# Kernel optimization log

Measured on AMD Instinct MI355X. Metric: run time of the kernel, lower is better.

The kernel has to match this reference:

```python
import jax, jax.numpy as jnp
import numpy as np

EPS = 1e-12  # torch F.normalize eps

def _l2norm(x):
    # matches torch.nn.functional.normalize(x, dim=-1): x / max(||x||, eps)
    n = jnp.sqrt(jnp.sum(x * x, axis=-1, keepdims=True))
    return x / jnp.maximum(n, EPS)

def setup_inputs() -> dict:
    key = jax.random.key(0)
    k1, k2, k3 = jax.random.split(key, 3)
    N, D, H, C = 4096, 16384, 256, 28
    return {
        "features": jax.random.normal(k1, (N, H), dtype=jnp.float32),
        "ex_features": jax.random.normal(k2, (D, H), dtype=jnp.float32),
        "ex_class_reps": jax.random.normal(k3, (D, C), dtype=jnp.float32),
        "p_factor": 3,
    }

def reference(features, ex_features, ex_class_reps, p_factor):
    # cosine similarity: [N, D]
    s = _l2norm(features) @ _l2norm(ex_features).T
    # power-law activation preserving sign
    a = jnp.sign(s) * jnp.abs(s) ** p_factor
    intensity = a.sum(axis=1)           # [N]
    echo = a @ ex_class_reps            # [N, C]
    return (echo, intensity)
```

## Files before the change

kernel.cpp:

```cpp
#include <hip/hip_runtime.h>
#include <cstdint>

#define HDIM 256
#define MT   128
#define BD   32
#define SPLITS 32

typedef short bf16x8 __attribute__((ext_vector_type(8)));
typedef short bf16x4 __attribute__((ext_vector_type(4)));
typedef float f32x4  __attribute__((ext_vector_type(4)));

typedef const __attribute__((address_space(1))) short as1_short;
typedef __attribute__((address_space(3))) short as3_short;

static __device__ __forceinline__ short f2bf(float x) {
    union { float f; uint32_t u; } v; v.f = x;
    uint32_t u = v.u;
    uint32_t r = (u + 0x7fffu + ((u >> 16) & 1u)) >> 16;
    return (short)r;
}

__global__ __launch_bounds__(256) void prep_kernel(const float* __restrict__ fsrc,
                                                   const float* __restrict__ esrc,
                                                   const float* __restrict__ reps,
                                                   short* __restrict__ dst,
                                                   short* __restrict__ rt,
                                                   int N, int rows_total,
                                                   int D, int C, int nb_nrm) {
    __shared__ float lds[128][29];
    const int tid = threadIdx.x;
    if ((int)blockIdx.x < nb_nrm) {
        int wv = tid >> 6;
        int lane = tid & 63;
        int row = blockIdx.x * 4 + wv;
        if (row >= rows_total) return;
        const float* src = (row < N) ? (fsrc + (size_t)row * HDIM)
                                     : (esrc + (size_t)(row - N) * HDIM);
        const float4 v = *(const float4*)(src + lane * 4);
        float ss = v.x * v.x + v.y * v.y + v.z * v.z + v.w * v.w;
        #pragma unroll
        for (int m = 1; m < 64; m <<= 1) ss += __shfl_xor(ss, m, 64);
        float scale = 1.0f / fmaxf(sqrtf(ss), 1e-12f);
        short4 o;
        o.x = f2bf(v.x * scale); o.y = f2bf(v.y * scale);
        o.z = f2bf(v.z * scale); o.w = f2bf(v.w * scale);
        int chunk = (lane >> 1) ^ (row & 7);
        *(short4*)(dst + (size_t)row * HDIM + chunk * 8 + (lane & 1) * 4) = o;
    } else {
        const int bx = blockIdx.x - nb_nrm;
        const int d0 = bx * 128;
        const int total = 128 * C;
        const float* src = reps + (size_t)d0 * C;
        for (int i = tid; i < total; i += 256)
            lds[i / C][i % C] = src[i];
        __syncthreads();
        const int c = tid >> 3;
        const int dsub = (tid & 7) * 16;
        short* dstp = rt + (size_t)c * D + d0 + dsub;
        #pragma unroll
        for (int j0 = 0; j0 < 16; j0 += 4) {
            short4 o;
            float v0, v1, v2, v3;
            if (c < C) {
                v0 = lds[dsub + j0 + 0][c]; v1 = lds[dsub + j0 + 1][c];
                v2 = lds[dsub + j0 + 2][c]; v3 = lds[dsub + j0 + 3][c];
            } else {
                float f = (c == C) ? 1.0f : 0.0f;
                v0 = v1 = v2 = v3 = f;
            }
            o.x = f2bf(v0); o.y = f2bf(v1); o.z = f2bf(v2); o.w = f2bf(v3);
            *(short4*)(dstp + j0) = o;
        }
    }
}

__global__ __launch_bounds__(256, 4) void fused_kernel(const short* __restrict__ Fn,
                                                       const short* __restrict__ En,
                                                       const short* __restrict__ Rt,
                                                       const int* __restrict__ pptr,
                                                       float* __restrict__ partial,
                                                       int N, int D, int C, int Dchunk) {
    __shared__ __align__(16) short lds_en[2][BD * HDIM];

    const int tid  = threadIdx.x;
    const int lane = tid & 63;
    const int wv   = tid >> 6;
    const int q    = lane >> 4;
    const int l    = lane & 15;
    const int p    = pptr[0];

    const int Mbase = blockIdx.y * MT;
    const int dbase = blockIdx.x * Dchunk;

    const f32x4 zf = {0.0f, 0.0f, 0.0f, 0.0f};

    bf16x8 afrag[2][8];
    #pragma unroll
    for (int fn = 0; fn < 2; ++fn) {
        const short* rowp = Fn + (size_t)(Mbase + wv * 32 + fn * 16 + l) * HDIM;
        #pragma unroll
        for (int ks = 0; ks < 8; ++ks)
            afrag[fn][ks] = *(const bf16x8*)(rowp + (((ks * 4 + q) ^ (l & 7)) << 3));
    }

    f32x4 echo_acc[2][2];
    echo_acc[0][0] = zf; echo_acc[0][1] = zf;
    echo_acc[1][0] = zf; echo_acc[1][1] = zf;

    const int iters = Dchunk / BD;

    #define STAGE(buf_, it_)                                                        \
        {                                                                           \
            const short* gbase = En + (size_t)(dbase + (it_) * BD) * HDIM + tid * 8;\
            _Pragma("unroll")                                                       \
            for (int i = 0; i < 4; ++i) {                                           \
                as3_short* lp = (as3_short*)(lds_en[buf_] + (i * 256 + wv * 64) * 8);\
                __builtin_amdgcn_global_load_lds((as1_short*)(gbase + i * 2048),    \
                                                 lp, 16, 0, 0);                     \
            }                                                                       \
        }

    STAGE(0, 0)

    const short* rtp = Rt + (size_t)l * D + q * 4;

    for (int it = 0; it < iters; ++it) {
        const int buf = it & 1;
        __syncthreads();
        if (it + 1 < iters) STAGE(buf ^ 1, it + 1)

        const int d0 = dbase + it * BD;

        f32x4 sT[2][2];
        sT[0][0] = zf; sT[0][1] = zf; sT[1][0] = zf; sT[1][1] = zf;
        #pragma unroll
        for (int ks = 0; ks < 8; ++ks) {
            #pragma unroll
            for (int en = 0; en < 2; ++en) {
                const int row  = en * 16 + l;
                const int slot = (ks * 4 + q) ^ (l & 7);
                bf16x8 ef = *(const bf16x8*)(lds_en[buf] + row * HDIM + slot * 8);
                sT[en][0] = __builtin_amdgcn_mfma_f32_16x16x32_bf16(ef, afrag[0][ks], sT[en][0], 0, 0, 0);
                sT[en][1] = __builtin_amdgcn_mfma_f32_16x16x32_bf16(ef, afrag[1][ks], sT[en][1], 0, 0, 0);
            }
        }

        bf16x4 pfrag[2][2];
        #pragma unroll
        for (int en = 0; en < 2; ++en) {
            #pragma unroll
            for (int fn = 0; fn < 2; ++fn) {
                bf16x4 pf;
                #pragma unroll
                for (int r = 0; r < 4; ++r) {
                    float sv = sT[en][fn][r];
                    float a;
                    if (p == 3)      a = sv * sv * sv;
                    else if (p == 1) a = sv;
                    else if (p == 2) a = sv * fabsf(sv);
                    else             a = copysignf(powf(fabsf(sv), (float)p), sv);
                    pf[r] = f2bf(a);
                }
                pfrag[fn][en] = pf;
            }
        }

        #pragma unroll
        for (int dblk = 0; dblk < 2; ++dblk) {
            const int doff = d0 + dblk * 16;
            bf16x4 rt0 = *(const bf16x4*)(rtp + doff);
            bf16x4 rt1 = *(const bf16x4*)(rtp + (size_t)16 * D + doff);
            #pragma unroll
            for (int fn = 0; fn < 2; ++fn) {
                echo_acc[fn][0] = __builtin_amdgcn_mfma_f32_16x16x16bf16_1k(rt0, pfrag[fn][dblk], echo_acc[fn][0], 0, 0, 0);
                echo_acc[fn][1] = __builtin_amdgcn_mfma_f32_16x16x16bf16_1k(rt1, pfrag[fn][dblk], echo_acc[fn][1], 0, 0, 0);
            }
        }
    }

    #pragma unroll
    for (int fn = 0; fn < 2; ++fn) {
        const int grow = Mbase + wv * 32 + fn * 16 + l;
        float* rowp = partial + ((size_t)blockIdx.x * N + grow) * 32 + q * 4;
        *(f32x4*)(rowp)      = echo_acc[fn][0];
        *(f32x4*)(rowp + 16) = echo_acc[fn][1];
    }
}

__global__ __launch_bounds__(256) void reduce_kernel(const float* __restrict__ partial,
                                                     float* __restrict__ echo,
                                                     float* __restrict__ inten,
                                                     int N, int splits, int C) {
    int t = blockIdx.x * 256 + threadIdx.x;
    int row = t >> 5, c = t & 31;
    if (row >= N || c > C) return;
    float s = 0.0f;
    for (int k = 0; k < splits; ++k)
        s += partial[((size_t)k * N + (size_t)row) * 32 + c];
    if (c < C) echo[(size_t)row * C + c] = s;
    else       inten[row] = s;
}

extern "C" void kernel_launch(void* const* d_in, const int* in_sizes, int n_in,
                              void* d_out, int out_size, void* d_ws, size_t ws_size,
                              hipStream_t stream) {
    const int N = in_sizes[0] / HDIM;
    const int D = in_sizes[1] / HDIM;
    const int C = in_sizes[2] / D;

    const float* feat = (const float*)d_in[0];
    const float* exf  = (const float*)d_in[1];
    const float* reps = (const float*)d_in[2];
    const int*   p    = (const int*)d_in[3];

    short* Fn = (short*)d_ws;
    short* En = Fn + (size_t)N * HDIM;
    short* Rt = En + (size_t)D * HDIM;
    float* partial = (float*)(Rt + (size_t)32 * D);

    float* echo  = (float*)d_out;
    float* inten = echo + (size_t)N * C;

    const int nb_nrm = (N + D) / 4;
    hipLaunchKernelGGL(prep_kernel, dim3(nb_nrm + D / 128), dim3(256), 0, stream,
                       feat, exf, reps, Fn, Rt, N, N + D, D, C, nb_nrm);

    const int Dchunk = D / SPLITS;
    hipLaunchKernelGGL(fused_kernel, dim3(SPLITS, N / MT), dim3(256), 0, stream,
                       Fn, En, Rt, p, partial, N, D, C, Dchunk);

    hipLaunchKernelGGL(reduce_kernel, dim3(N * 32 / 256), dim3(256), 0, stream,
                       partial, echo, inten, N, SPLITS, C);
}
```

Baseline: 144.1 us.

## Software-pipeline first GEMM with activation and echo MFMA across iterations

Restructures the main loop so the similarity GEMM for tile i runs alongside the activation and echo MFMAs for tile i-1, using two score register sets in ping-pong fashion. The loop is unrolled by two with fixed LDS buffers, and the Rt fragment loads are issued before the activation. This is meant to hide MFMA dependency latency and the global Rt load latency behind independent work. In exchange it raises register pressure and assumes an even iteration count of at least two, which holds when Dchunk/BD is even.

```diff
diff --git a/kernel.cpp b/kernel.cpp
--- a/kernel.cpp
+++ b/kernel.cpp
@@ -120,63 +120,88 @@
             }                                                                       \
         }
 
+    #define GEMM1(BUF_, ST_)                                                        \
+        {                                                                           \
+            ST_[0][0] = zf; ST_[0][1] = zf; ST_[1][0] = zf; ST_[1][1] = zf;         \
+            _Pragma("unroll")                                                       \
+            for (int ks = 0; ks < 8; ++ks) {                                        \
+                _Pragma("unroll")                                                   \
+                for (int en = 0; en < 2; ++en) {                                    \
+                    const int row  = en * 16 + l;                                   \
+                    const int slot = (ks * 4 + q) ^ (l & 7);                        \
+                    bf16x8 ef = *(const bf16x8*)(lds_en[BUF_] + row * HDIM + slot * 8); \
+                    ST_[en][0] = __builtin_amdgcn_mfma_f32_16x16x32_bf16(ef, afrag[0][ks], ST_[en][0], 0, 0, 0); \
+                    ST_[en][1] = __builtin_amdgcn_mfma_f32_16x16x32_bf16(ef, afrag[1][ks], ST_[en][1], 0, 0, 0); \
+                }                                                                   \
+            }                                                                       \
+        }
+
+    #define ACT2(ST_, IT_)                                                          \
+        {                                                                           \
+            const int d0p = dbase + (IT_) * BD;                                     \
+            bf16x4 rt_f[2][2];                                                      \
+            _Pragma("unroll")                                                       \
+            for (int dblk = 0; dblk < 2; ++dblk) {                                  \
+                const int doff = d0p + dblk * 16;                                   \
+                rt_f[dblk][0] = *(const bf16x4*)(rtp + doff);                       \
+                rt_f[dblk][1] = *(const bf16x4*)(rtp + (size_t)16 * D + doff);      \
+            }                                                                       \
+            bf16x4 pfrag[2][2];                                                     \
+            _Pragma("unroll")                                                       \
+            for (int en = 0; en < 2; ++en) {                                        \
+                _Pragma("unroll")                                                   \
+                for (int fn = 0; fn < 2; ++fn) {                                    \
+                    bf16x4 pf;                                                      \
+                    _Pragma("unroll")                                               \
+                    for (int r = 0; r < 4; ++r) {                                   \
+                        float sv = ST_[en][fn][r];                                  \
+                        float a;                                                    \
+                        if (p == 3)      a = sv * sv * sv;                          \
+                        else if (p == 1) a = sv;                                    \
+                        else if (p == 2) a = sv * fabsf(sv);                        \
+                        else             a = copysignf(powf(fabsf(sv), (float)p), sv); \
+                        pf[r] = f2bf(a);                                            \
+                    }                                                               \
+                    pfrag[fn][en] = pf;                                             \
+                }                                                                   \
+            }                                                                       \
+            _Pragma("unroll")                                                       \
+            for (int dblk = 0; dblk < 2; ++dblk) {                                  \
+                _Pragma("unroll")                                                   \
+                for (int fn = 0; fn < 2; ++fn) {                                    \
+                    echo_acc[fn][0] = __builtin_amdgcn_mfma_f32_16x16x16bf16_1k(rt_f[dblk][0], pfrag[fn][dblk], echo_acc[fn][0], 0, 0, 0); \
+                    echo_acc[fn][1] = __builtin_amdgcn_mfma_f32_16x16x16bf16_1k(rt_f[dblk][1], pfrag[fn][dblk], echo_acc[fn][1], 0, 0, 0); \
+                }                                                                   \
+            }                                                                       \
+        }
+
+    const short* rtp = Rt + (size_t)l * D + q * 4;
+
+    f32x4 sTa[2][2];
+    f32x4 sTb[2][2];
+
     STAGE(0, 0)
-
-    const short* rtp = Rt + (size_t)l * D + q * 4;
-
-    for (int it = 0; it < iters; ++it) {
-        const int buf = it & 1;
+    __syncthreads();
+    STAGE(1, 1)
+    GEMM1(0, sTa)
+
+    __syncthreads();
+    STAGE(0, 2)
+    GEMM1(1, sTb)
+    ACT2(sTa, 0)
+
+    for (int it = 2; it < iters; it += 2) {
         __syncthreads();
-        if (it + 1 < iters) STAGE(buf ^ 1, it + 1)
-
-        const int d0 = dbase + it * BD;
-
-        f32x4 sT[2][2];
-        sT[0][0] = zf; sT[0][1] = zf; sT[1][0] = zf; sT[1][1] = zf;
-        #pragma unroll
-        for (int ks = 0; ks < 8; ++ks) {
-            #pragma unroll
-            for (int en = 0; en < 2; ++en) {
-                const int row  = en * 16 + l;
-                const int slot = (ks * 4 + q) ^ (l & 7);
-                bf16x8 ef = *(const bf16x8*)(lds_en[buf] + row * HDIM + slot * 8);
-                sT[en][0] = __builtin_amdgcn_mfma_f32_16x16x32_bf16(ef, afrag[0][ks], sT[en][0], 0, 0, 0);
-                sT[en][1] = __builtin_amdgcn_mfma_f32_16x16x32_bf16(ef, afrag[1][ks], sT[en][1], 0, 0, 0);
-            }
-        }
-
-        bf16x4 pfrag[2][2];
-        #pragma unroll
-        for (int en = 0; en < 2; ++en) {
-            #pragma unroll
-            for (int fn = 0; fn < 2; ++fn) {
-                bf16x4 pf;
-                #pragma unroll
-                for (int r = 0; r < 4; ++r) {
-                    float sv = sT[en][fn][r];
-                    float a;
-                    if (p == 3)      a = sv * sv * sv;
-                    else if (p == 1) a = sv;
-                    else if (p == 2) a = sv * fabsf(sv);
-                    else             a = copysignf(powf(fabsf(sv), (float)p), sv);
-                    pf[r] = f2bf(a);
-                }
-                pfrag[fn][en] = pf;
-            }
-        }
-
-        #pragma unroll
-        for (int dblk = 0; dblk < 2; ++dblk) {
-            const int doff = d0 + dblk * 16;
-            bf16x4 rt0 = *(const bf16x4*)(rtp + doff);
-            bf16x4 rt1 = *(const bf16x4*)(rtp + (size_t)16 * D + doff);
-            #pragma unroll
-            for (int fn = 0; fn < 2; ++fn) {
-                echo_acc[fn][0] = __builtin_amdgcn_mfma_f32_16x16x16bf16_1k(rt0, pfrag[fn][dblk], echo_acc[fn][0], 0, 0, 0);
-                echo_acc[fn][1] = __builtin_amdgcn_mfma_f32_16x16x16bf16_1k(rt1, pfrag[fn][dblk], echo_acc[fn][1], 0, 0, 0);
-            }
-        }
-    }
+        if (it + 1 < iters) STAGE(1, it + 1)
+        GEMM1(0, sTa)
+        ACT2(sTb, it - 1)
+
+        __syncthreads();
+        if (it + 2 < iters) STAGE(0, it + 2)
+        GEMM1(1, sTb)
+        ACT2(sTa, it)
+    }
+    ACT2(sTb, iters - 1)
 
     #pragma unroll
     for (int fn = 0; fn < 2; ++fn) {
@@ -185,6 +210,10 @@
         *(f32x4*)(rowp)      = echo_acc[fn][0];
         *(f32x4*)(rowp + 16) = echo_acc[fn][1];
     }
+
+    #undef STAGE
+    #undef GEMM1
+    #undef ACT2
 }
 
 __global__ __launch_bounds__(256) void reduce_kernel(const float* __restrict__ partial,
```

New measurement: 198.0 us. +37.4%, slower.

## Replace split-K partial buffer and reduce kernel with atomic accumulation into output

Applied to the files above, without the earlier changes.

Drops the partial-sum workspace and the separate reduce kernel. The fused kernel now adds its split-D results straight into echo and intensity with float atomicAdd, and extra blocks in the prep kernel zero the output first. The inner loop is also reordered so each 16-wide D block runs its similarity MFMAs, power activation and echo MFMAs together, which shortens live ranges of the sT accumulators. In exchange it adds about 32 split contributions of atomic traffic per output element, and the float sums are no longer deterministic in order.

```diff
diff --git a/kernel.cpp b/kernel.cpp
--- a/kernel.cpp
+++ b/kernel.cpp
@@ -5,6 +5,7 @@
 #define MT   128
 #define BD   32
 #define SPLITS 32
+#define ZB   32
 
 typedef short bf16x8 __attribute__((ext_vector_type(8)));
 typedef short bf16x4 __attribute__((ext_vector_type(4)));
@@ -25,6 +26,8 @@
                                                    const float* __restrict__ reps,
                                                    short* __restrict__ dst,
                                                    short* __restrict__ rt,
+                                                   float* __restrict__ outbuf,
+                                                   int out_f4,
                                                    int N, int rows_total,
                                                    int D, int C, int nb_nrm) {
     __shared__ float lds[128][29];
@@ -46,7 +49,7 @@
         o.z = f2bf(v.z * scale); o.w = f2bf(v.w * scale);
         int chunk = (lane >> 1) ^ (row & 7);
         *(short4*)(dst + (size_t)row * HDIM + chunk * 8 + (lane & 1) * 4) = o;
-    } else {
+    } else if ((int)blockIdx.x < nb_nrm + D / 128) {
         const int bx = blockIdx.x - nb_nrm;
         const int d0 = bx * 128;
         const int total = 128 * C;
@@ -71,6 +74,12 @@
             o.x = f2bf(v0); o.y = f2bf(v1); o.z = f2bf(v2); o.w = f2bf(v3);
             *(short4*)(dstp + j0) = o;
         }
+    } else {
+        const int zb = blockIdx.x - nb_nrm - D / 128;
+        const f32x4 z4 = {0.0f, 0.0f, 0.0f, 0.0f};
+        f32x4* out4 = (f32x4*)outbuf;
+        for (int i = zb * 256 + tid; i < out_f4; i += ZB * 256)
+            out4[i] = z4;
     }
 }
 
@@ -78,7 +87,8 @@
                                                        const short* __restrict__ En,
                                                        const short* __restrict__ Rt,
                                                        const int* __restrict__ pptr,
-                                                       float* __restrict__ partial,
+                                                       float* __restrict__ echo,
+                                                       float* __restrict__ inten,
                                                        int N, int D, int C, int Dchunk) {
     __shared__ __align__(16) short lds_en[2][BD * HDIM];
 
@@ -131,49 +141,44 @@
 
         const int d0 = dbase + it * BD;
 
-        f32x4 sT[2][2];
-        sT[0][0] = zf; sT[0][1] = zf; sT[1][0] = zf; sT[1][1] = zf;
-        #pragma unroll
-        for (int ks = 0; ks < 8; ++ks) {
-            #pragma unroll
-            for (int en = 0; en < 2; ++en) {
+        #pragma unroll
+        for (int en = 0; en < 2; ++en) {
+            const int doff = d0 + en * 16;
+            bf16x4 rt0 = *(const bf16x4*)(rtp + doff);
+            bf16x4 rt1 = *(const bf16x4*)(rtp + (size_t)16 * D + doff);
+
+            f32x4 s0 = zf, s1 = zf;
+            #pragma unroll
+            for (int ks = 0; ks < 8; ++ks) {
                 const int row  = en * 16 + l;
                 const int slot = (ks * 4 + q) ^ (l & 7);
                 bf16x8 ef = *(const bf16x8*)(lds_en[buf] + row * HDIM + slot * 8);
-                sT[en][0] = __builtin_amdgcn_mfma_f32_16x16x32_bf16(ef, afrag[0][ks], sT[en][0], 0, 0, 0);
-                sT[en][1] = __builtin_amdgcn_mfma_f32_16x16x32_bf16(ef, afrag[1][ks], sT[en][1], 0, 0, 0);
-            }
-        }
-
-        bf16x4 pfrag[2][2];
-        #pragma unroll
-        for (int en = 0; en < 2; ++en) {
+                s0 = __builtin_amdgcn_mfma_f32_16x16x32_bf16(ef, afrag[0][ks], s0, 0, 0, 0);
+                s1 = __builtin_amdgcn_mfma_f32_16x16x32_bf16(ef, afrag[1][ks], s1, 0, 0, 0);
+            }
+
+            bf16x4 pf[2];
             #pragma unroll
             for (int fn = 0; fn < 2; ++fn) {
-                bf16x4 pf;
+                const f32x4& sv4 = (fn == 0) ? s0 : s1;
+                bf16x4 pfv;
                 #pragma unroll
                 for (int r = 0; r < 4; ++r) {
-                    float sv = sT[en][fn][r];
+                    float sv = sv4[r];
                     float a;
                     if (p == 3)      a = sv * sv * sv;
                     else if (p == 1) a = sv;
                     else if (p == 2) a = sv * fabsf(sv);
                     else             a = copysignf(powf(fabsf(sv), (float)p), sv);
-                    pf[r] = f2bf(a);
+                    pfv[r] = f2bf(a);
                 }
-                pfrag[fn][en] = pf;
-            }
-        }
-
-        #pragma unroll
-        for (int dblk = 0; dblk < 2; ++dblk) {
-            const int doff = d0 + dblk * 16;
-            bf16x4 rt0 = *(const bf16x4*)(rtp + doff);
-            bf16x4 rt1 = *(const bf16x4*)(rtp + (size_t)16 * D + doff);
+                pf[fn] = pfv;
+            }
+
             #pragma unroll
             for (int fn = 0; fn < 2; ++fn) {
-                echo_acc[fn][0] = __builtin_amdgcn_mfma_f32_16x16x16bf16_1k(rt0, pfrag[fn][dblk], echo_acc[fn][0], 0, 0, 0);
-                echo_acc[fn][1] = __builtin_amdgcn_mfma_f32_16x16x16bf16_1k(rt1, pfrag[fn][dblk], echo_acc[fn][1], 0, 0, 0);
+                echo_acc[fn][0] = __builtin_amdgcn_mfma_f32_16x16x16bf16_1k(rt0, pf[fn], echo_acc[fn][0], 0, 0, 0);
+                echo_acc[fn][1] = __builtin_amdgcn_mfma_f32_16x16x16bf16_1k(rt1, pf[fn], echo_acc[fn][1], 0, 0, 0);
             }
         }
     }
@@ -181,24 +186,19 @@
     #pragma unroll
     for (int fn = 0; fn < 2; ++fn) {
         const int grow = Mbase + wv * 32 + fn * 16 + l;
-        float* rowp = partial + ((size_t)blockIdx.x * N + grow) * 32 + q * 4;
-        *(f32x4*)(rowp)      = echo_acc[fn][0];
-        *(f32x4*)(rowp + 16) = echo_acc[fn][1];
-    }
-}
-
-__global__ __launch_bounds__(256) void reduce_kernel(const float* __restrict__ partial,
-                                                     float* __restrict__ echo,
-                                                     float* __restrict__ inten,
-                                                     int N, int splits, int C) {
-    int t = blockIdx.x * 256 + threadIdx.x;
-    int row = t >> 5, c = t & 31;
-    if (row >= N || c > C) return;
-    float s = 0.0f;
-    for (int k = 0; k < splits; ++k)
-        s += partial[((size_t)k * N + (size_t)row) * 32 + c];
-    if (c < C) echo[(size_t)row * C + c] = s;
-    else       inten[row] = s;
+        #pragma unroll
+        for (int ct = 0; ct < 2; ++ct) {
+            #pragma unroll
+            for (int r = 0; r < 4; ++r) {
+                const int c = ct * 16 + q * 4 + r;
+                const float v = echo_acc[fn][ct][r];
+                if (c < C)       atomicAdd(echo + (size_t)grow * C + c, v);
+                else if (c == C) atomicAdd(inten + grow, v);
+            }
+        }
+    }
+
+    #undef STAGE
 }
 
 extern "C" void kernel_launch(void* const* d_in, const int* in_sizes, int n_in,
@@ -216,19 +216,17 @@
     short* Fn = (short*)d_ws;
     short* En = Fn + (size_t)N * HDIM;
     short* Rt = En + (size_t)D * HDIM;
-    float* partial = (float*)(Rt + (size_t)32 * D);
 
     float* echo  = (float*)d_out;
     float* inten = echo + (size_t)N * C;
+    const int out_f4 = (N * C + N) / 4;
 
     const int nb_nrm = (N + D) / 4;
-    hipLaunchKernelGGL(prep_kernel, dim3(nb_nrm + D / 128), dim3(256), 0, stream,
-                       feat, exf, reps, Fn, Rt, N, N + D, D, C, nb_nrm);
+    hipLaunchKernelGGL(prep_kernel, dim3(nb_nrm + D / 128 + ZB), dim3(256), 0, stream,
+                       feat, exf, reps, Fn, Rt, (float*)d_out, out_f4,
+                       N, N + D, D, C, nb_nrm);
 
     const int Dchunk = D / SPLITS;
     hipLaunchKernelGGL(fused_kernel, dim3(SPLITS, N / MT), dim3(256), 0, stream,
-                       Fn, En, Rt, p, partial, N, D, C, Dchunk);
-
-    hipLaunchKernelGGL(reduce_kernel, dim3(N * 32 / 256), dim3(256), 0, stream,
-                       partial, echo, inten, N, SPLITS, C);
-}
+                       Fn, En, Rt, p, echo, inten, N, D, C, Dchunk);
+}
```

New measurement: 248.5 us. +72.4%, slower.
